# Kernel tuning notes

Hardware: AMD Instinct MI355X
Metric: run time of the kernel (lower is better)

The kernel has to match this reference:

```python
import jax, jax.numpy as jnp
import numpy as np

N = 10000           # nodes
E = 320000          # edges
H = 128             # hidden_channels
L = 4               # num_layers
NUM_GRAPHS = 64
NUM_CLASSES = 10
MSG_EPS = 1e-7      # GENConv message epsilon


def layer_norm(x, g, b, eps=1e-5):
    mu = x.mean(-1, keepdims=True)
    var = x.var(-1, keepdims=True)
    return (x - mu) / jnp.sqrt(var + eps) * g + b


def setup_inputs() -> dict:
    key = jax.random.key(0)
    ks = jax.random.split(key, 10)
    def rn(k, shape, scale=0.05):
        return jax.random.normal(k, shape, jnp.float32) * scale
    return {
        "x": jax.random.normal(ks[0], (N, H), jnp.float32),
        "edge_attr": jax.random.normal(ks[1], (E, H), jnp.float32),
        "enc_W": rn(ks[2], (H, H)), "enc_b": jnp.zeros((H,), jnp.float32),
        "t": jnp.ones((L,), jnp.float32),                      # learnable softmax temperature per GENConv
        "W1": rn(ks[3], (L, H, 2 * H)), "b1": jnp.zeros((L, 2 * H), jnp.float32),
        "mlp_ln_g": jnp.ones((L, 2 * H), jnp.float32), "mlp_ln_b": jnp.zeros((L, 2 * H), jnp.float32),
        "W2": rn(ks[4], (L, 2 * H, H)), "b2": jnp.zeros((L, H), jnp.float32),
        "ln_g": jnp.ones((L, H), jnp.float32), "ln_b": jnp.zeros((L, H), jnp.float32),
        "lin_W": rn(ks[5], (H, NUM_CLASSES)), "lin_b": jnp.zeros((NUM_CLASSES,), jnp.float32),
        "edge_index": jax.random.randint(ks[6], (2, E), 0, N),
        "batch": jnp.sort(jax.random.randint(ks[7], (N,), 0, NUM_GRAPHS)),
    }


def genconv(x, src, dst, edge_attr, t, W1, b1, g1, be1, W2, b2):
    # GENConv, aggr='softmax': msg = relu(x_j + e) + eps; scatter-softmax over dst
    m = jax.nn.relu(x[src] + edge_attr) + MSG_EPS          # [E, H]
    logit = m * t
    mx = jax.ops.segment_max(logit, dst, num_segments=N)   # [N, H]
    ex = jnp.exp(logit - mx[dst])
    den = jax.ops.segment_sum(ex, dst, num_segments=N)
    alpha = ex / den[dst]                                   # per-edge softmax weight
    agg = jax.ops.segment_sum(m * alpha, dst, num_segments=N)  # [N, H]
    h = agg + x                                             # root skip inside GENConv
    # MLP: Lin(H,2H) -> LayerNorm -> ReLU -> Lin(2H,H)
    h = jax.nn.relu(layer_norm(h @ W1 + b1, g1, be1))
    return h @ W2 + b2


def reference(x, edge_attr, enc_W, enc_b, t, W1, b1, mlp_ln_g, mlp_ln_b, W2, b2, ln_g, ln_b, lin_W, lin_b, edge_index, batch):
    src, dst = edge_index[0], edge_index[1]
    h = x @ enc_W + enc_b
    # layers[0]: conv only
    h = genconv(h, src, dst, edge_attr, t[0], W1[0], b1[0], mlp_ln_g[0], mlp_ln_b[0], W2[0], b2[0])
    # layers[1:]: res+ block  x = x + conv(dropout(act(norm(x))))  (dropout=eval identity)
    for i in range(1, L):
        r = jax.nn.relu(layer_norm(h, ln_g[i], ln_b[i]))
        h = h + genconv(r, src, dst, edge_attr, t[i], W1[i], b1[i], mlp_ln_g[i], mlp_ln_b[i], W2[i], b2[i])
    h = jax.nn.relu(layer_norm(h, ln_g[0], ln_b[0]))       # layers[0].act(layers[0].norm(x))
    pooled = jax.ops.segment_sum(h, batch, num_segments=NUM_GRAPHS)  # global_add_pool
    return pooled @ lin_W + lin_b, pooled
```

## Files before the change

### kernel.cpp

```cpp
#include <hip/hip_runtime.h>
#include <hip/hip_bf16.h>

#define N_NODES 10000
#define N_EDGES 320000
#define H 128
#define H2 256
#define NLAYERS 4
#define NG 64
#define NC 10
#define MSG_EPS 1e-7f
#define LN_EPS 1e-5f

typedef __attribute__((ext_vector_type(8))) short bf16x8;
typedef __attribute__((ext_vector_type(4))) float f32x4;

__device__ __forceinline__ short f2bf(float f) {
    union { float f; unsigned u; } x; x.f = f;
    unsigned r = x.u + 0x7FFFu + ((x.u >> 16) & 1u);
    return (short)(r >> 16);
}


__global__ __launch_bounds__(256) void count_kernel(const int* __restrict__ dst,
                                                    int* __restrict__ counts) {
    int e = blockIdx.x * 256 + threadIdx.x;
    if (e < N_EDGES) atomicAdd(&counts[dst[e]], 1);
}

__global__ __launch_bounds__(256) void scan_kernel(const int* __restrict__ counts,
                                                   int* __restrict__ off,
                                                   int* __restrict__ cursor) {
    __shared__ int part[256];
    int tid = threadIdx.x;
    const int CH = (N_NODES + 255) / 256;
    int base = tid * CH;
    int s = 0;
    for (int i = 0; i < CH; ++i) {
        int idx = base + i;
        if (idx < N_NODES) s += counts[idx];
    }
    part[tid] = s;
    __syncthreads();
    for (int d = 1; d < 256; d <<= 1) {
        int t = (tid >= d) ? part[tid - d] : 0;
        __syncthreads();
        part[tid] += t;
        __syncthreads();
    }
    int run = part[tid] - s;
    for (int i = 0; i < CH; ++i) {
        int idx = base + i;
        if (idx < N_NODES) {
            off[idx] = run;
            cursor[idx] = run;
            run += counts[idx];
        }
    }
    if (tid == 255) off[N_NODES] = run;
}

__global__ __launch_bounds__(256) void scatter_kernel(const int* __restrict__ src,
                                                      const int* __restrict__ dst,
                                                      int* __restrict__ cursor,
                                                      int* __restrict__ perm_e,
                                                      int* __restrict__ perm_s) {
    int e = blockIdx.x * 256 + threadIdx.x;
    if (e < N_EDGES) {
        int p = atomicAdd(&cursor[dst[e]], 1);
        perm_e[p] = e;
        perm_s[p] = src[e];
    }
}


__global__ __launch_bounds__(256) void wconv_kernel(const float* __restrict__ W1,
                                                    const float* __restrict__ W2,
                                                    short* __restrict__ W1T,
                                                    short* __restrict__ W2T) {
    int idx = blockIdx.x * 256 + threadIdx.x;
    if (idx < NLAYERS * H * H2) {
        int k = idx & (H - 1);
        int c = (idx >> 7) & (H2 - 1);
        int l = idx >> 15;
        W1T[idx] = f2bf(W1[l * H * H2 + k * H2 + c]);
        int k2 = idx & (H2 - 1);
        int c2 = (idx >> 8) & (H - 1);
        W2T[idx] = f2bf(W2[l * H * H2 + k2 * H + c2]);
    }
}


__global__ __launch_bounds__(128) void encoder_kernel(const float* __restrict__ x,
                                                      const float* __restrict__ W,
                                                      const float* __restrict__ b,
                                                      float* __restrict__ h) {
    __shared__ float sx[8][H];
    int v0 = blockIdx.x * 8;
    int tid = threadIdx.x;
    for (int idx = tid; idx < 8 * H; idx += 128)
        sx[idx >> 7][idx & 127] = x[v0 * H + idx];
    __syncthreads();
    float y[8] = {0.f, 0.f, 0.f, 0.f, 0.f, 0.f, 0.f, 0.f};
    for (int k = 0; k < H; ++k) {
        float w = W[k * H + tid];
#pragma unroll
        for (int n = 0; n < 8; ++n) y[n] += sx[n][k] * w;
    }
    float bb = b[tid];
#pragma unroll
    for (int n = 0; n < 8; ++n) h[(v0 + n) * H + tid] = y[n] + bb;
}


__global__ __launch_bounds__(256) void ln_relu_kernel(const float* __restrict__ h,
                                                      const float* __restrict__ g,
                                                      const float* __restrict__ b,
                                                      float* __restrict__ out,
                                                      const int* __restrict__ batch,
                                                      float* __restrict__ pooled,
                                                      int do_pool) {
    int wave = threadIdx.x >> 6, lane = threadIdx.x & 63;
    int v = blockIdx.x * 4 + wave;
    if (v >= N_NODES) return;
    float2 x = ((const float2*)(h + (size_t)v * H))[lane];
    float s = x.x + x.y, sq = x.x * x.x + x.y * x.y;
    for (int d = 32; d; d >>= 1) {
        s += __shfl_down(s, d);
        sq += __shfl_down(sq, d);
    }
    s = __shfl(s, 0);
    sq = __shfl(sq, 0);
    float mu = s * (1.f / H);
    float var = sq * (1.f / H) - mu * mu;
    float rstd = rsqrtf(var + LN_EPS);
    float2 gg = ((const float2*)g)[lane];
    float2 bb = ((const float2*)b)[lane];
    float f0 = fmaxf((x.x - mu) * rstd * gg.x + bb.x, 0.f);
    float f1 = fmaxf((x.y - mu) * rstd * gg.y + bb.y, 0.f);
    if (do_pool) {
        float* p = pooled + (size_t)batch[v] * H + lane * 2;
        atomicAdd(p, f0);
        atomicAdd(p + 1, f1);
    } else {
        ((float2*)(out + (size_t)v * H))[lane] = make_float2(f0, f1);
    }
}


#define PROC(cc)                                           \
    {                                                      \
        float m = fmaxf(xv.cc + ev.cc, 0.f) + MSG_EPS;     \
        float exx = __expf(m * tl);                        \
        den.cc += exx;                                     \
        num.cc += m * exx;                                 \
    }

__global__ __launch_bounds__(256) void edge_agg_kernel(const float* __restrict__ xcur,
                                                       const float* __restrict__ ea,
                                                       const int* __restrict__ off,
                                                       const int* __restrict__ perm_e,
                                                       const int* __restrict__ perm_s,
                                                       const float* __restrict__ t, int l,
                                                       float* __restrict__ u) {
    int v = blockIdx.x;
    int tid = threadIdx.x;
    int g = tid >> 5;
    int lane = tid & 31;
    float tl = t[l];
    int b = off[v], e_end = off[v + 1];
    const float4* x4 = (const float4*)xcur;
    const float4* e4 = (const float4*)ea;
    float4 den = {0.f, 0.f, 0.f, 0.f}, num = {0.f, 0.f, 0.f, 0.f};

    int i = b + g;
    for (; i + 24 < e_end; i += 32) {
        int e0 = perm_e[i],      s0 = perm_s[i];
        int e1 = perm_e[i + 8],  s1 = perm_s[i + 8];
        int e2 = perm_e[i + 16], s2 = perm_s[i + 16];
        int e3 = perm_e[i + 24], s3 = perm_s[i + 24];
        float4 xv0 = x4[(size_t)s0 * 32 + lane], ev0 = e4[(size_t)e0 * 32 + lane];
        float4 xv1 = x4[(size_t)s1 * 32 + lane], ev1 = e4[(size_t)e1 * 32 + lane];
        float4 xv2 = x4[(size_t)s2 * 32 + lane], ev2 = e4[(size_t)e2 * 32 + lane];
        float4 xv3 = x4[(size_t)s3 * 32 + lane], ev3 = e4[(size_t)e3 * 32 + lane];
        { float4 xv = xv0, ev = ev0; PROC(x) PROC(y) PROC(z) PROC(w) }
        { float4 xv = xv1, ev = ev1; PROC(x) PROC(y) PROC(z) PROC(w) }
        { float4 xv = xv2, ev = ev2; PROC(x) PROC(y) PROC(z) PROC(w) }
        { float4 xv = xv3, ev = ev3; PROC(x) PROC(y) PROC(z) PROC(w) }
    }
    for (; i < e_end; i += 8) {
        int e0 = perm_e[i], s0 = perm_s[i];
        float4 xv = x4[(size_t)s0 * 32 + lane];
        float4 ev = e4[(size_t)e0 * 32 + lane];
        PROC(x) PROC(y) PROC(z) PROC(w)
    }

    __shared__ float4 sden[8][32];
    __shared__ float4 snum[8][32];
    sden[g][lane] = den;
    snum[g][lane] = num;
    __syncthreads();
#pragma unroll
    for (int step = 4; step >= 1; step >>= 1) {
        if (g < step) {
            float4 a = sden[g][lane], b2 = sden[g + step][lane];
            a.x += b2.x; a.y += b2.y; a.z += b2.z; a.w += b2.w;
            sden[g][lane] = a;
            float4 c = snum[g][lane], d2 = snum[g + step][lane];
            c.x += d2.x; c.y += d2.y; c.z += d2.z; c.w += d2.w;
            snum[g][lane] = c;
        }
        __syncthreads();
    }
    if (g == 0) {
        float4 dn = sden[0][lane], nm = snum[0][lane];
        float4 xv = x4[(size_t)v * 32 + lane];
        float4 o;
        o.x = (dn.x > 0.f ? nm.x / dn.x : 0.f) + xv.x;
        o.y = (dn.y > 0.f ? nm.y / dn.y : 0.f) + xv.y;
        o.z = (dn.z > 0.f ? nm.z / dn.z : 0.f) + xv.z;
        o.w = (dn.w > 0.f ? nm.w / dn.w : 0.f) + xv.w;
        ((float4*)u)[(size_t)v * 32 + lane] = o;
    }
}


__global__ __launch_bounds__(256) void mlp_mfma_kernel(const float* __restrict__ u,
                                                       const float* __restrict__ hin,
                                                       float* __restrict__ hout,
                                                       const short* __restrict__ W1T,
                                                       const float* __restrict__ b1,
                                                       const float* __restrict__ g1,
                                                       const float* __restrict__ be1,
                                                       const short* __restrict__ W2T,
                                                       const float* __restrict__ b2,
                                                       int residual) {
    __shared__ short Ub[32 * 128];
    __shared__ short Ab[32 * 256];
    __shared__ float redv[2][32][4];
    __shared__ float musig[2][32];
    int tid = threadIdx.x;
    int wave = tid >> 6, lane = tid & 63;
    int l15 = lane & 15, lg = lane >> 4;
    int v0 = blockIdx.x * 32;
    int nrow = N_NODES - v0; if (nrow > 32) nrow = 32;

    for (int c = tid; c < 32 * 16; c += 256) {
        int row = c >> 4, ch = c & 15;
        bf16x8 val = {0, 0, 0, 0, 0, 0, 0, 0};
        if (row < nrow) {
            const float4* up = (const float4*)(u + (size_t)(v0 + row) * H + ch * 8);
            float4 f0 = up[0], f1 = up[1];
            val[0] = f2bf(f0.x); val[1] = f2bf(f0.y); val[2] = f2bf(f0.z); val[3] = f2bf(f0.w);
            val[4] = f2bf(f1.x); val[5] = f2bf(f1.y); val[6] = f2bf(f1.z); val[7] = f2bf(f1.w);
        }
        *(bf16x8*)&Ub[row * 128 + ((ch ^ (row & 7)) * 8)] = val;
    }
    __syncthreads();

    int nc0 = wave * 64;
    f32x4 acc[2][4];
#pragma unroll
    for (int mi = 0; mi < 2; ++mi)
#pragma unroll
        for (int ni = 0; ni < 4; ++ni) acc[mi][ni] = (f32x4){0.f, 0.f, 0.f, 0.f};
#pragma unroll
    for (int ks = 0; ks < 4; ++ks) {
        bf16x8 af[2], bfr[4];
#pragma unroll
        for (int mi = 0; mi < 2; ++mi) {
            int row = mi * 16 + l15;
            int ch = ks * 4 + lg;
            af[mi] = *(const bf16x8*)&Ub[row * 128 + ((ch ^ (row & 7)) * 8)];
        }
#pragma unroll
        for (int ni = 0; ni < 4; ++ni) {
            int col = nc0 + ni * 16 + l15;
            bfr[ni] = *(const bf16x8*)&W1T[col * H + ks * 32 + lg * 8];
        }
#pragma unroll
        for (int mi = 0; mi < 2; ++mi)
#pragma unroll
            for (int ni = 0; ni < 4; ++ni)
                acc[mi][ni] = __builtin_amdgcn_mfma_f32_16x16x32_bf16(af[mi], bfr[ni], acc[mi][ni], 0, 0, 0);
    }

    float bcol[4];
#pragma unroll
    for (int ni = 0; ni < 4; ++ni) bcol[ni] = b1[nc0 + ni * 16 + l15];
#pragma unroll
    for (int mi = 0; mi < 2; ++mi) {
#pragma unroll
        for (int j = 0; j < 4; ++j) {
            float s = 0.f, q = 0.f;
#pragma unroll
            for (int ni = 0; ni < 4; ++ni) {
                float y = acc[mi][ni][j] + bcol[ni];
                acc[mi][ni][j] = y;
                s += y;
                q += y * y;
            }
#pragma unroll
            for (int m = 8; m >= 1; m >>= 1) {
                s += __shfl_xor(s, m);
                q += __shfl_xor(q, m);
            }
            if (l15 == 0) {
                int row = mi * 16 + lg * 4 + j;
                redv[0][row][wave] = s;
                redv[1][row][wave] = q;
            }
        }
    }
    __syncthreads();
    if (tid < 32) {
        float S = redv[0][tid][0] + redv[0][tid][1] + redv[0][tid][2] + redv[0][tid][3];
        float Q = redv[1][tid][0] + redv[1][tid][1] + redv[1][tid][2] + redv[1][tid][3];
        float mu = S * (1.f / H2);
        float var = Q * (1.f / H2) - mu * mu;
        musig[0][tid] = mu;
        musig[1][tid] = rsqrtf(var + LN_EPS);
    }
    __syncthreads();

    float gcol[4], becol[4];
#pragma unroll
    for (int ni = 0; ni < 4; ++ni) {
        gcol[ni] = g1[nc0 + ni * 16 + l15];
        becol[ni] = be1[nc0 + ni * 16 + l15];
    }
#pragma unroll
    for (int mi = 0; mi < 2; ++mi)
#pragma unroll
        for (int j = 0; j < 4; ++j) {
            int row = mi * 16 + lg * 4 + j;
            float mu = musig[0][row], rs = musig[1][row];
#pragma unroll
            for (int ni = 0; ni < 4; ++ni) {
                int col = nc0 + ni * 16 + l15;
                float a = fmaxf((acc[mi][ni][j] - mu) * rs * gcol[ni] + becol[ni], 0.f);
                int ch = col >> 3, o8 = col & 7;
                Ab[row * 256 + ((ch ^ (row & 7)) * 8) + o8] = f2bf(a);
            }
        }
    __syncthreads();

    int nc2 = wave * 32;
    f32x4 acc2[2][2];
#pragma unroll
    for (int mi = 0; mi < 2; ++mi)
#pragma unroll
        for (int ni = 0; ni < 2; ++ni) acc2[mi][ni] = (f32x4){0.f, 0.f, 0.f, 0.f};
#pragma unroll
    for (int ks = 0; ks < 8; ++ks) {
        bf16x8 af[2], bfr[2];
#pragma unroll
        for (int mi = 0; mi < 2; ++mi) {
            int row = mi * 16 + l15;
            int ch = ks * 4 + lg;
            af[mi] = *(const bf16x8*)&Ab[row * 256 + ((ch ^ (row & 7)) * 8)];
        }
#pragma unroll
        for (int ni = 0; ni < 2; ++ni) {
            int col = nc2 + ni * 16 + l15;
            bfr[ni] = *(const bf16x8*)&W2T[col * H2 + ks * 32 + lg * 8];
        }
#pragma unroll
        for (int mi = 0; mi < 2; ++mi)
#pragma unroll
            for (int ni = 0; ni < 2; ++ni)
                acc2[mi][ni] = __builtin_amdgcn_mfma_f32_16x16x32_bf16(af[mi], bfr[ni], acc2[mi][ni], 0, 0, 0);
    }

#pragma unroll
    for (int ni = 0; ni < 2; ++ni) {
        int col = nc2 + ni * 16 + l15;
        float bb = b2[col];
#pragma unroll
        for (int mi = 0; mi < 2; ++mi)
#pragma unroll
            for (int j = 0; j < 4; ++j) {
                int row = mi * 16 + lg * 4 + j;
                if (row < nrow) {
                    size_t gi = (size_t)(v0 + row) * H + col;
                    float z = acc2[mi][ni][j] + bb;
                    hout[gi] = residual ? hin[gi] + z : z;
                }
            }
    }
}


__global__ __launch_bounds__(640) void logits_kernel(const float* __restrict__ pooled,
                                                     const float* __restrict__ W,
                                                     const float* __restrict__ b,
                                                     float* __restrict__ out) {
    int tid = threadIdx.x;
    if (tid < NG * NC) {
        int g = tid / NC, c = tid % NC;
        float acc = b[c];
        for (int k = 0; k < H; ++k) acc += pooled[g * H + k] * W[k * NC + c];
        out[g * NC + c] = acc;
    }
    for (int idx = tid; idx < NG * H; idx += 640) out[NG * NC + idx] = pooled[idx];
}


extern "C" void kernel_launch(void* const* d_in, const int* in_sizes, int n_in,
                              void* d_out, int out_size, void* d_ws, size_t ws_size,
                              hipStream_t stream) {
    const float* x     = (const float*)d_in[0];
    const float* ea    = (const float*)d_in[1];
    const float* enc_W = (const float*)d_in[2];
    const float* enc_b = (const float*)d_in[3];
    const float* t     = (const float*)d_in[4];
    const float* W1    = (const float*)d_in[5];
    const float* b1    = (const float*)d_in[6];
    const float* g1    = (const float*)d_in[7];
    const float* be1   = (const float*)d_in[8];
    const float* W2    = (const float*)d_in[9];
    const float* b2    = (const float*)d_in[10];
    const float* lng   = (const float*)d_in[11];
    const float* lnb   = (const float*)d_in[12];
    const float* linW  = (const float*)d_in[13];
    const float* linb  = (const float*)d_in[14];
    const int*   ei    = (const int*)d_in[15];
    const int*   batch = (const int*)d_in[16];
    const int* src = ei;
    const int* dst = ei + N_EDGES;
    float* out = (float*)d_out;

    short* W1T = (short*)d_ws;
    short* W2T = W1T + NLAYERS * H * H2;
    float* h      = (float*)(W2T + NLAYERS * H * H2);
    float* r      = h + (size_t)N_NODES * H;
    float* u      = r + (size_t)N_NODES * H;
    float* pooled = u + (size_t)N_NODES * H;
    int* counts = (int*)(pooled + NG * H);
    int* off    = counts + N_NODES;
    int* cursor = off + N_NODES + 16;
    int* perm_e = cursor + N_NODES;
    int* perm_s = perm_e + N_EDGES;

    hipMemsetAsync(counts, 0, N_NODES * sizeof(int), stream);
    hipMemsetAsync(pooled, 0, NG * H * sizeof(float), stream);

    count_kernel<<<(N_EDGES + 255) / 256, 256, 0, stream>>>(dst, counts);
    scan_kernel<<<1, 256, 0, stream>>>(counts, off, cursor);
    scatter_kernel<<<(N_EDGES + 255) / 256, 256, 0, stream>>>(src, dst, cursor, perm_e, perm_s);
    wconv_kernel<<<(NLAYERS * H * H2 + 255) / 256, 256, 0, stream>>>(W1, W2, W1T, W2T);

    encoder_kernel<<<N_NODES / 8, 128, 0, stream>>>(x, enc_W, enc_b, h);

    for (int l = 0; l < NLAYERS; ++l) {
        const float* xcur;
        if (l == 0) {
            xcur = h;
        } else {
            ln_relu_kernel<<<(N_NODES + 3) / 4, 256, 0, stream>>>(h, lng + l * H, lnb + l * H, r,
                                                                  nullptr, nullptr, 0);
            xcur = r;
        }
        edge_agg_kernel<<<N_NODES, 256, 0, stream>>>(xcur, ea, off, perm_e, perm_s, t, l, u);
        mlp_mfma_kernel<<<(N_NODES + 31) / 32, 256, 0, stream>>>(
            u, h, h, W1T + (size_t)l * H * H2, b1 + l * H2, g1 + l * H2, be1 + l * H2,
            W2T + (size_t)l * H * H2, b2 + l * H, l > 0);
    }

    ln_relu_kernel<<<(N_NODES + 3) / 4, 256, 0, stream>>>(h, lng, lnb, nullptr, batch, pooled, 1);
    logits_kernel<<<1, 640, 0, stream>>>(pooled, linW, linb, out);
}
```

Baseline: 614.9 us.

## Pre-permute edge attributes into dst-sorted bf16 buffer for edge aggregation

Adds a one-time kernel that gathers edge_attr in CSR (dst-sorted) order and stores it as bf16, so each layer's edge aggregation reads edge features contiguously at half the bytes and no longer needs the perm_e indirection. This targets the dominant per-layer memory traffic of streaming the 164 MB fp32 edge_attr four times. The cost is an extra full pass over edge_attr plus a write of the 82 MB bf16 copy, more workspace, and reduced precision in the edge features.

```diff
diff --git a/kernel.cpp b/kernel.cpp
--- a/kernel.cpp
+++ b/kernel.cpp
@@ -18,6 +18,15 @@
     union { float f; unsigned u; } x; x.f = f;
     unsigned r = x.u + 0x7FFFu + ((x.u >> 16) & 1u);
     return (short)(r >> 16);
+}
+__device__ __forceinline__ unsigned short f2bfu(float f) {
+    union { float f; unsigned u; } x; x.f = f;
+    unsigned r = x.u + 0x7FFFu + ((x.u >> 16) & 1u);
+    return (unsigned short)(r >> 16);
+}
+__device__ __forceinline__ float bf2f(unsigned short u) {
+    union { unsigned u; float f; } x; x.u = ((unsigned)u) << 16;
+    return x.f;
 }
 
 
@@ -69,6 +78,21 @@
         int p = atomicAdd(&cursor[dst[e]], 1);
         perm_e[p] = e;
         perm_s[p] = src[e];
+    }
+}
+
+
+__global__ __launch_bounds__(256) void permute_ea_kernel(const float* __restrict__ ea,
+                                                         const int* __restrict__ perm_e,
+                                                         ushort* __restrict__ eap) {
+    int g = threadIdx.x >> 5, lane = threadIdx.x & 31;
+    int i = blockIdx.x * 8 + g;
+    if (i < N_EDGES) {
+        int e = perm_e[i];
+        float4 v = ((const float4*)ea)[(size_t)e * 32 + lane];
+        ushort4 o;
+        o.x = f2bfu(v.x); o.y = f2bfu(v.y); o.z = f2bfu(v.z); o.w = f2bfu(v.w);
+        ((ushort4*)eap)[(size_t)i * 32 + lane] = o;
     }
 }
 
@@ -155,10 +179,13 @@
         num.cc += m * exx;                                 \
     }
 
+__device__ __forceinline__ float4 bf4(ushort4 u) {
+    return make_float4(bf2f(u.x), bf2f(u.y), bf2f(u.z), bf2f(u.w));
+}
+
 __global__ __launch_bounds__(256) void edge_agg_kernel(const float* __restrict__ xcur,
-                                                       const float* __restrict__ ea,
+                                                       const ushort* __restrict__ eap,
                                                        const int* __restrict__ off,
-                                                       const int* __restrict__ perm_e,
                                                        const int* __restrict__ perm_s,
                                                        const float* __restrict__ t, int l,
                                                        float* __restrict__ u) {
@@ -169,28 +196,29 @@
     float tl = t[l];
     int b = off[v], e_end = off[v + 1];
     const float4* x4 = (const float4*)xcur;
-    const float4* e4 = (const float4*)ea;
+    const ushort4* e4 = (const ushort4*)eap;
     float4 den = {0.f, 0.f, 0.f, 0.f}, num = {0.f, 0.f, 0.f, 0.f};
 
     int i = b + g;
     for (; i + 24 < e_end; i += 32) {
-        int e0 = perm_e[i],      s0 = perm_s[i];
-        int e1 = perm_e[i + 8],  s1 = perm_s[i + 8];
-        int e2 = perm_e[i + 16], s2 = perm_s[i + 16];
-        int e3 = perm_e[i + 24], s3 = perm_s[i + 24];
-        float4 xv0 = x4[(size_t)s0 * 32 + lane], ev0 = e4[(size_t)e0 * 32 + lane];
-        float4 xv1 = x4[(size_t)s1 * 32 + lane], ev1 = e4[(size_t)e1 * 32 + lane];
-        float4 xv2 = x4[(size_t)s2 * 32 + lane], ev2 = e4[(size_t)e2 * 32 + lane];
-        float4 xv3 = x4[(size_t)s3 * 32 + lane], ev3 = e4[(size_t)e3 * 32 + lane];
-        { float4 xv = xv0, ev = ev0; PROC(x) PROC(y) PROC(z) PROC(w) }
-        { float4 xv = xv1, ev = ev1; PROC(x) PROC(y) PROC(z) PROC(w) }
-        { float4 xv = xv2, ev = ev2; PROC(x) PROC(y) PROC(z) PROC(w) }
-        { float4 xv = xv3, ev = ev3; PROC(x) PROC(y) PROC(z) PROC(w) }
+        int s0 = perm_s[i], s1 = perm_s[i + 8], s2 = perm_s[i + 16], s3 = perm_s[i + 24];
+        float4 xv0 = x4[(size_t)s0 * 32 + lane];
+        ushort4 eb0 = e4[(size_t)i * 32 + lane];
+        float4 xv1 = x4[(size_t)s1 * 32 + lane];
+        ushort4 eb1 = e4[(size_t)(i + 8) * 32 + lane];
+        float4 xv2 = x4[(size_t)s2 * 32 + lane];
+        ushort4 eb2 = e4[(size_t)(i + 16) * 32 + lane];
+        float4 xv3 = x4[(size_t)s3 * 32 + lane];
+        ushort4 eb3 = e4[(size_t)(i + 24) * 32 + lane];
+        { float4 xv = xv0, ev = bf4(eb0); PROC(x) PROC(y) PROC(z) PROC(w) }
+        { float4 xv = xv1, ev = bf4(eb1); PROC(x) PROC(y) PROC(z) PROC(w) }
+        { float4 xv = xv2, ev = bf4(eb2); PROC(x) PROC(y) PROC(z) PROC(w) }
+        { float4 xv = xv3, ev = bf4(eb3); PROC(x) PROC(y) PROC(z) PROC(w) }
     }
     for (; i < e_end; i += 8) {
-        int e0 = perm_e[i], s0 = perm_s[i];
+        int s0 = perm_s[i];
         float4 xv = x4[(size_t)s0 * 32 + lane];
-        float4 ev = e4[(size_t)e0 * 32 + lane];
+        float4 ev = bf4(e4[(size_t)i * 32 + lane]);
         PROC(x) PROC(y) PROC(z) PROC(w)
     }
 
@@ -429,9 +457,10 @@
     const int* dst = ei + N_EDGES;
     float* out = (float*)d_out;
 
-    short* W1T = (short*)d_ws;
-    short* W2T = W1T + NLAYERS * H * H2;
-    float* h      = (float*)(W2T + NLAYERS * H * H2);
+    short* W1T   = (short*)d_ws;
+    short* W2T   = W1T + NLAYERS * H * H2;
+    ushort* eap  = (ushort*)(W2T + NLAYERS * H * H2);
+    float* h     = (float*)(eap + (size_t)N_EDGES * H);
     float* r      = h + (size_t)N_NODES * H;
     float* u      = r + (size_t)N_NODES * H;
     float* pooled = u + (size_t)N_NODES * H;
@@ -447,6 +476,7 @@
     count_kernel<<<(N_EDGES + 255) / 256, 256, 0, stream>>>(dst, counts);
     scan_kernel<<<1, 256, 0, stream>>>(counts, off, cursor);
     scatter_kernel<<<(N_EDGES + 255) / 256, 256, 0, stream>>>(src, dst, cursor, perm_e, perm_s);
+    permute_ea_kernel<<<N_EDGES / 8, 256, 0, stream>>>(ea, perm_e, eap);
     wconv_kernel<<<(NLAYERS * H * H2 + 255) / 256, 256, 0, stream>>>(W1, W2, W1T, W2T);
 
     encoder_kernel<<<N_NODES / 8, 128, 0, stream>>>(x, enc_W, enc_b, h);
@@ -460,7 +490,7 @@
                                                                   nullptr, nullptr, 0);
             xcur = r;
         }
-        edge_agg_kernel<<<N_NODES, 256, 0, stream>>>(xcur, ea, off, perm_e, perm_s, t, l, u);
+        edge_agg_kernel<<<N_NODES, 256, 0, stream>>>(xcur, eap, off, perm_s, t, l, u);
         mlp_mfma_kernel<<<(N_NODES + 31) / 32, 256, 0, stream>>>(
             u, h, h, W1T + (size_t)l * H * H2, b1 + l * H2, g1 + l * H2, be1 + l * H2,
             W2T + (size_t)l * H * H2, b2 + l * H, l > 0);
```

New measurement: 612.5 us. About the same (-0.4%).
